# Performance work log

Measured on AMD Instinct MI355X. Metric: run time of the kernel, lower is better.

Reference implementation:

```python
import jax, jax.numpy as jnp
import numpy as np

D = 1024
H = 8
HD = D // H
SCALE = HD ** -0.5


def setup_inputs() -> dict:
    key = jax.random.key(0)
    ks = jax.random.split(key, 12)
    s = 0.02
    return {
        "x": jax.random.normal(ks[0], (4, 2048, D), dtype=jnp.float32),
        "attn_mask": jax.random.randint(ks[1], (2048, 2048), 0, 2, dtype=jnp.int32),
        "qkv_w": jax.random.normal(ks[2], (3 * D, D), dtype=jnp.float32) * s,
        "qkv_b": jnp.zeros((3 * D,), dtype=jnp.float32),
        "q_w": jax.random.normal(ks[3], (D, D), dtype=jnp.float32) * s,
        "q_b": jnp.zeros((D,), dtype=jnp.float32),
        "k_w": jax.random.normal(ks[4], (D, D), dtype=jnp.float32) * s,
        "k_b": jnp.zeros((D,), dtype=jnp.float32),
        "v_w": jax.random.normal(ks[5], (D, D), dtype=jnp.float32) * s,
        "v_b": jnp.zeros((D,), dtype=jnp.float32),
        "out_w": jax.random.normal(ks[6], (D, D), dtype=jnp.float32) * s,
        "out_b": jnp.zeros((D,), dtype=jnp.float32),
    }


def reference(x, attn_mask, qkv_w, qkv_b, q_w, q_b, k_w, k_b, v_w, v_b, out_w, out_b):
    B, S, _ = x.shape
    qkv = x @ qkv_w.T + qkv_b
    q, k, v = jnp.split(qkv, 3, axis=-1)
    # per-stream multi-head projections, then split heads: [B,H,S,HD]
    def heads(t, w, b):
        return (t @ w.T + b).reshape(B, S, H, HD).transpose(0, 2, 1, 3)
    q = heads(q, q_w, q_b)
    k = heads(k, k_w, k_b)
    v = heads(v, v_w, v_b)
    # scaled dot-product attention with masked softmax
    scores = jnp.einsum("bhqd,bhkd->bhqk", q, k) * SCALE
    scores = jnp.where(attn_mask == 1, -jnp.inf, scores)
    attn = jax.nn.softmax(scores, axis=-1)
    o = jnp.einsum("bhqk,bhkd->bhqd", attn, v)
    o = o.transpose(0, 2, 1, 3).reshape(B, S, D)
    return o @ out_w.T + out_b
```

## Files before the change

kernel.cpp:

```cpp
#include <hip/hip_runtime.h>
#include <stdint.h>

typedef unsigned short u16;
typedef unsigned int u32;
typedef unsigned long long u64;
using f32x4 = __attribute__((ext_vector_type(4))) float;
using f32x16 = __attribute__((ext_vector_type(16))) float;
using s16x8 = __attribute__((ext_vector_type(8))) short;
using u16x4 = __attribute__((ext_vector_type(4))) unsigned short;
using u32x4 = __attribute__((ext_vector_type(4))) u32;

static constexpr float kQScale = (float)(0.08838834764831845 * 1.4426950408889634);

__device__ __forceinline__ u16 f2bf(float f) {
  uint32_t u = __float_as_uint(f);
  u += 0x7fffu + ((u >> 16) & 1u);
  return (u16)(u >> 16);
}

__device__ __forceinline__ float fexp2(float x) {
#if __has_builtin(__builtin_amdgcn_exp2f)
  return __builtin_amdgcn_exp2f(x);
#else
  return exp2f(x);
#endif
}

__device__ __forceinline__ u32 cvtpk(float lo, float hi) {
  u32 r;
  asm("v_cvt_pk_bf16_f32 %0, %1, %2" : "=v"(r) : "v"(lo), "v"(hi));
  return r;
}

__device__ __forceinline__ void mfma16(f32x4& d, s16x8 a, s16x8 b) {
  asm volatile("v_mfma_f32_16x16x32_bf16 %0, %1, %2, %0" : "+v"(d) : "v"(a), "v"(b));
}
__device__ __forceinline__ void mfma32(f32x16& d, s16x8 a, s16x8 b) {
  asm volatile("v_mfma_f32_32x32x16_bf16 %0, %1, %2, %0" : "+v"(d) : "v"(a), "v"(b));
}

__device__ __forceinline__ void g2lds16(const void* g, void* l) {
  __builtin_amdgcn_global_load_lds(
      (__attribute__((address_space(1))) void*)(uintptr_t)g,
      (__attribute__((address_space(3))) void*)(uint32_t)(uintptr_t)l, 16, 0, 0);
}

__global__ __launch_bounds__(256) void cvt_f32_bf16(const float* __restrict__ in,
                                                    u16* __restrict__ out, int n) {
  int i = (blockIdx.x * 256 + threadIdx.x) * 4;
  if (i + 3 < n) {
    f32x4 v = *(const f32x4*)(in + i);
    u16x4 o = {f2bf(v.x), f2bf(v.y), f2bf(v.z), f2bf(v.w)};
    *(u16x4*)(out + i) = o;
  }
}

__global__ __launch_bounds__(256) void cvt4(const float* __restrict__ a, const float* __restrict__ b,
                                            const float* __restrict__ c, const float* __restrict__ d,
                                            u16* __restrict__ out) {
  int z = blockIdx.y;
  const float* in = z == 0 ? a : z == 1 ? b : z == 2 ? c : d;
  int i = (blockIdx.x * 256 + threadIdx.x) * 4;
  f32x4 v = *(const f32x4*)(in + i);
  u16x4 o = {f2bf(v.x), f2bf(v.y), f2bf(v.z), f2bf(v.w)};
  *(u16x4*)(out + (size_t)z * 1048576 + i) = o;
}

__global__ __launch_bounds__(256) void transpose_f32_bf16(const float* __restrict__ in,
                                                          u16* __restrict__ out, int R, int C) {
  __shared__ u16 tile[32][33];
  int bx = blockIdx.x, by = blockIdx.y;
  int tx = threadIdx.x & 31, ty = threadIdx.x >> 5;
#pragma unroll
  for (int k = 0; k < 4; ++k)
    tile[ty + k * 8][tx] = f2bf(in[(size_t)(by * 32 + ty + k * 8) * C + bx * 32 + tx]);
  __syncthreads();
#pragma unroll
  for (int k = 0; k < 4; ++k)
    out[(size_t)(bx * 32 + ty + k * 8) * R + by * 32 + tx] = tile[tx][ty + k * 8];
}

__global__ __launch_bounds__(256) void cbias3(const float* __restrict__ qw, const float* __restrict__ kw,
                                              const float* __restrict__ vw, const float* __restrict__ qkvb,
                                              const float* __restrict__ qb, const float* __restrict__ kb,
                                              const float* __restrict__ vb, float* __restrict__ out) {
  int z = blockIdx.y;
  const float* w = z == 0 ? qw : (z == 1 ? kw : vw);
  const float* ba = z == 0 ? qb : (z == 1 ? kb : vb);
  const float* bi = qkvb + z * 1024;
  int o = blockIdx.x * 4 + (threadIdx.x >> 6);
  int lane = threadIdx.x & 63;
  float s = 0.f;
  for (int m = lane; m < 1024; m += 64) s += w[o * 1024 + m] * bi[m];
#pragma unroll
  for (int d = 1; d < 64; d <<= 1) s += __shfl_xor(s, d);
  if (lane == 0) {
    float fin = s + ba[o];
    if (z == 0) fin *= kQScale;
    out[z * 1024 + o] = fin;
  }
}

__global__ __launch_bounds__(256) void pack_mask(const int* __restrict__ m, u64* __restrict__ pm) {
  int row = blockIdx.x;
  int wv = threadIdx.x >> 6, lane = threadIdx.x & 63;
#pragma unroll
  for (int i = 0; i < 8; ++i) {
    int word = wv * 8 + i;
    u64 b = __ballot(m[(size_t)row * 2048 + word * 64 + lane] == 1);
    if (lane == 0) pm[(size_t)row * 32 + word] = b;
  }
}

template <typename OUT_T, bool BIAS_PER_ROW>
__global__ __launch_bounds__(256, 2) void gemm_nt(const u16* __restrict__ A, int lda, long bsA,
                                                  const u16* __restrict__ B, int ldb, long bsB,
                                                  OUT_T* __restrict__ C, int ldc, long bsC,
                                                  const float* __restrict__ bias, long bsBias,
                                                  int NtilesN, int K, float scale_z0) {
  __shared__ __align__(16) u16 As[128 * 64];
  __shared__ __align__(16) u16 Bs[128 * 64];
  const int z = blockIdx.z;
  const float sc = (z == 0) ? scale_z0 : 1.f;
  A += (size_t)z * bsA; B += (size_t)z * bsB; C += (size_t)z * bsC;
  if (bias) bias += (size_t)z * bsBias;
  const int tm = blockIdx.x / NtilesN, tn = blockIdx.x % NtilesN;
  const int tid = threadIdx.x, lane = tid & 63, w = tid >> 6;
  const int wm = w >> 1, wn = w & 1;
  const int q = lane & 15, g = lane >> 4;
  f32x4 acc[4][4] = {};

  const u16* Ab = A + (size_t)(tm * 128 + (tid >> 3)) * lda + ((tid & 7) << 3);
  const u16* Bb = B + (size_t)(tn * 128 + (tid >> 3)) * ldb + ((tid & 7) << 3);
  char* AsW = (char*)As + (w << 10);
  char* BsW = (char*)Bs + (w << 10);

  for (int k0 = 0; k0 < K; k0 += 64) {
#pragma unroll
    for (int it = 0; it < 4; ++it) {
      g2lds16(Ab + (size_t)(it * 32) * lda + k0, AsW + it * 4096);
      g2lds16(Bb + (size_t)(it * 32) * ldb + k0, BsW + it * 4096);
    }
    __syncthreads();
#pragma unroll
    for (int kk = 0; kk < 2; ++kk) {
      s16x8 af[4], bf[4];
#pragma unroll
      for (int i = 0; i < 4; ++i)
        af[i] = *(const s16x8*)((const char*)As + (wm * 64 + i * 16 + q) * 128 + kk * 64 + g * 16);
#pragma unroll
      for (int i = 0; i < 4; ++i)
        bf[i] = *(const s16x8*)((const char*)Bs + (wn * 64 + i * 16 + q) * 128 + kk * 64 + g * 16);
#pragma unroll
      for (int mf = 0; mf < 4; ++mf)
#pragma unroll
        for (int nf = 0; nf < 4; ++nf) mfma16(acc[mf][nf], af[mf], bf[nf]);
    }
    __syncthreads();
  }
  asm volatile("s_nop 7\n\ts_nop 7");
#pragma unroll
  for (int mf = 0; mf < 4; ++mf)
#pragma unroll
    for (int nf = 0; nf < 4; ++nf) {
      const int row = tm * 128 + wm * 64 + mf * 16 + g * 4;
      const int col = tn * 128 + wn * 64 + nf * 16 + q;
      float bc = (!BIAS_PER_ROW && bias) ? bias[col] : 0.f;
#pragma unroll
      for (int r = 0; r < 4; ++r) {
        float v = acc[mf][nf][r] * sc;
        if (bias) v += BIAS_PER_ROW ? bias[row + r] : bc;
        if constexpr (sizeof(OUT_T) == 2)
          C[(size_t)(row + r) * ldc + col] = (OUT_T)f2bf(v);
        else
          C[(size_t)(row + r) * ldc + col] = (OUT_T)v;
      }
    }
}

__global__ __launch_bounds__(256, 2) void attn_fwd(const u16* __restrict__ Qb, const u16* __restrict__ Kb,
                                                   const u16* __restrict__ Vt, const u64* __restrict__ pmask,
                                                   u16* __restrict__ Ob) {
  __shared__ __align__(16) char K_lds[2 * 16384];
  __shared__ __align__(16) char V_lds[2 * 16384];
  __shared__ float l_red[4][32];
  const int n = blockIdx.x;
  const int slot = n >> 3;
  const int grp = (n & 7) * 4 + (slot >> 4);
  const int qt = slot & 15;
  const int h = grp & 7, b = grp >> 3;
  const int tid = threadIdx.x, w = tid >> 6, lane = tid & 63;
  const int ql = lane & 31;
  const int hi = lane >> 5;
  const int q0 = qt * 128;

  s16x8 qf[8];
  const u16* qrow = Qb + (size_t)(b * 2048 + q0 + w * 32 + ql) * 1024 + h * 128 + 8 * hi;
#pragma unroll
  for (int kd = 0; kd < 8; ++kd) qf[kd] = *(const s16x8*)(qrow + 16 * kd);

  f32x16 oacc[4] = {};
  float lp = 0.f;

  const int ksr = tid >> 4, ksc = tid & 15;
  const int vsr = tid >> 3, vsc = tid & 7;
  const int sw = ql & 15;

  auto stageKV = [&](int buf, int s2) {
    const int kv0 = s2 * 64;
    char* kb = K_lds + buf * 16384 + (w << 10);
    char* vb = V_lds + buf * 16384 + (w << 10);
#pragma unroll
    for (int it = 0; it < 4; ++it) {
      int kr = it * 16 + ksr;
      g2lds16(Kb + (size_t)(b * 2048 + kv0 + kr) * 1024 + h * 128 + ((ksc ^ (kr & 15)) << 3),
              kb + it * 4096);
      int vr = it * 32 + vsr;
      g2lds16(Vt + (size_t)(h * 128 + vr) * 8192 + b * 2048 + kv0 + ((vsc ^ (vr & 7)) << 3),
              vb + it * 4096);
    }
  };

  stageKV(0, 0);
  __syncthreads();

  for (int s = 0; s < 32; ++s) {
    const int cur = s & 1;
    if (s + 1 < 32) stageKV(cur ^ 1, s + 1);
    const char* Kc = K_lds + cur * 16384;
    const char* Vc = V_lds + cur * 16384;

    u64 pw = pmask[(size_t)(q0 + w * 32 + ql) * 32 + s];

    f32x16 sacc0 = {}, sacc1 = {};
    __builtin_amdgcn_s_setprio(1);
#pragma unroll
    for (int kd = 0; kd < 8; ++kd) {
      int c = (2 * kd + hi) ^ sw;
      s16x8 kf0 = *(const s16x8*)(Kc + ql * 256 + (c << 4));
      s16x8 kf1 = *(const s16x8*)(Kc + (32 + ql) * 256 + (c << 4));
      mfma32(sacc0, kf0, qf[kd]);
      mfma32(sacc1, kf1, qf[kd]);
    }
    __builtin_amdgcn_s_setprio(0);
    asm volatile("s_nop 7\n\ts_nop 7");

    u32 Wp[8][2];
#pragma unroll
    for (int nt = 0; nt < 2; ++nt) {
      u32 halfm = ((u32)(pw >> (32 * nt))) >> (4 * hi);
#pragma unroll
      for (int t = 0; t < 4; ++t) {
        float e[4];
#pragma unroll
        for (int j = 0; j < 4; ++j) {
          float ev = fexp2((nt == 0 ? sacc0[4 * t + j] : sacc1[4 * t + j]) - 16.f);
          if ((halfm >> (8 * t + j)) & 1u) ev = 0.f;
          e[j] = ev;
          lp += ev;
        }
        Wp[nt * 4 + t][0] = cvtpk(e[0], e[1]);
        Wp[nt * 4 + t][1] = cvtpk(e[2], e[3]);
      }
    }

    s16x8 pa[4];
#pragma unroll
    for (int ks = 0; ks < 4; ++ks) {
      u32 s0 = hi ? Wp[2 * ks][0] : Wp[2 * ks + 1][0];
      u32 s1 = hi ? Wp[2 * ks][1] : Wp[2 * ks + 1][1];
      u32 r0 = (u32)__shfl_xor((int)s0, 32);
      u32 r1 = (u32)__shfl_xor((int)s1, 32);
      u32 o0 = hi ? Wp[2 * ks + 1][0] : Wp[2 * ks][0];
      u32 o1 = hi ? Wp[2 * ks + 1][1] : Wp[2 * ks][1];
      u32x4 wv;
      wv.x = hi ? r0 : o0;
      wv.y = hi ? r1 : o1;
      wv.z = hi ? o0 : r0;
      wv.w = hi ? o1 : r1;
      pa[ks] = __builtin_bit_cast(s16x8, wv);
    }
    asm volatile("s_nop 3");

    __builtin_amdgcn_s_setprio(1);
#pragma unroll
    for (int ks = 0; ks < 4; ++ks) {
#pragma unroll
      for (int dt = 0; dt < 4; ++dt) {
        int vrow = dt * 32 + ql;
        s16x8 vf = *(const s16x8*)(Vc + vrow * 128 + ((((2 * ks + hi)) ^ (vrow & 7)) << 4));
        mfma32(oacc[dt], pa[ks], vf);
      }
    }
    __builtin_amdgcn_s_setprio(0);
    __syncthreads();
  }

  asm volatile("s_nop 7\n\ts_nop 7");
  lp += __shfl_xor(lp, 32);
  if (lane < 32) l_red[w][lane] = 1.f / lp;
  float rl[16];
#pragma unroll
  for (int reg = 0; reg < 16; ++reg)
    rl[reg] = l_red[w][(reg & 3) + 8 * (reg >> 2) + 4 * hi];
#pragma unroll
  for (int dt = 0; dt < 4; ++dt)
#pragma unroll
    for (int reg = 0; reg < 16; ++reg) {
      int qr = (reg & 3) + 8 * (reg >> 2) + 4 * hi;
      size_t trow = (size_t)(b * 2048 + q0 + w * 32 + qr);
      Ob[trow * 1024 + h * 128 + dt * 32 + ql] = f2bf(oacc[dt][reg] * rl[reg]);
    }
}

extern "C" void kernel_launch(void* const* d_in, const int* in_sizes, int n_in,
                              void* d_out, int out_size, void* d_ws, size_t ws_size,
                              hipStream_t stream) {
  (void)in_sizes; (void)n_in; (void)out_size; (void)ws_size;
  const float* x    = (const float*)d_in[0];
  const int*   am   = (const int*)d_in[1];
  const float* qkvw = (const float*)d_in[2];
  const float* qkvb = (const float*)d_in[3];
  const float* qw   = (const float*)d_in[4];
  const float* qb   = (const float*)d_in[5];
  const float* kw   = (const float*)d_in[6];
  const float* kb   = (const float*)d_in[7];
  const float* vw   = (const float*)d_in[8];
  const float* vb   = (const float*)d_in[9];
  const float* ow   = (const float*)d_in[10];
  const float* ob   = (const float*)d_in[11];

  char* p = (char*)d_ws;
  auto take = [&](size_t n) { char* r = p; p += (n + 255) & ~(size_t)255; return r; };
  u16* xb    = (u16*)take(8192ull * 1024 * 2);
  u16* qkvwT = (u16*)take(1024ull * 3072 * 2);
  u16* wb4   = (u16*)take(4ull * 1048576 * 2);
  u16* comb3 = (u16*)take(3ull * 1048576 * 2);
  float* cb3 = (float*)take(3ull * 1024 * 4);
  u16* QK2   = (u16*)take(2ull * 8192 * 1024 * 2);
  u16* V2t   = (u16*)take(8192ull * 1024 * 2);
  u64* pm    = (u64*)take(2048ull * 32 * 8);
  u16* Obuf  = xb;

  cvt_f32_bf16<<<8192, 256, 0, stream>>>(x, xb, 8192 * 1024);
  cvt4<<<dim3(1024, 4), 256, 0, stream>>>(qw, kw, vw, ow, wb4);
  transpose_f32_bf16<<<dim3(32, 96), 256, 0, stream>>>(qkvw, qkvwT, 3072, 1024);
  cbias3<<<dim3(256, 3), 256, 0, stream>>>(qw, kw, vw, qkvb, qb, kb, vb, cb3);

  gemm_nt<u16, false><<<dim3(64, 1, 3), 256, 0, stream>>>(
      wb4, 1024, 1048576, qkvwT, 3072, 1024, comb3, 1024, 1048576, nullptr, 0, 8, 1024, kQScale);
  gemm_nt<u16, false><<<dim3(512, 1, 2), 256, 0, stream>>>(
      xb, 1024, 0, comb3, 1024, 1048576, QK2, 1024, 8192ll * 1024, cb3, 1024, 8, 1024, 1.f);
  gemm_nt<u16, true><<<dim3(512, 1, 1), 256, 0, stream>>>(
      comb3 + 2 * 1048576, 1024, 0, xb, 1024, 0, V2t, 8192, 0, cb3 + 2048, 0, 64, 1024, 1.f);

  pack_mask<<<2048, 256, 0, stream>>>(am, pm);
  attn_fwd<<<512, 256, 0, stream>>>(QK2, QK2 + 8192ull * 1024, V2t, pm, Obuf);

  gemm_nt<float, false><<<dim3(512, 1, 1), 256, 0, stream>>>(
      Obuf, 1024, 0, wb4 + 3 * 1048576, 1024, 0, (float*)d_out, 1024, 0, ob, 0, 8, 1024, 1.f);
}
```

Before: 261.6 us.

## Add 256x256 GEMM for fused QK projection and compute row sums with MFMA

```diff
diff --git a/kernel.cpp b/kernel.cpp
--- a/kernel.cpp
+++ b/kernel.cpp
@@ -38,12 +38,19 @@
 __device__ __forceinline__ void mfma32(f32x16& d, s16x8 a, s16x8 b) {
   asm volatile("v_mfma_f32_32x32x16_bf16 %0, %1, %2, %0" : "+v"(d) : "v"(a), "v"(b));
 }
+__device__ __forceinline__ f32x16 mfma32_z(s16x8 a, s16x8 b) {
+  f32x16 d;
+  asm volatile("v_mfma_f32_32x32x16_bf16 %0, %1, %2, 0" : "=&v"(d) : "v"(a), "v"(b));
+  return d;
+}
 
 __device__ __forceinline__ void g2lds16(const void* g, void* l) {
   __builtin_amdgcn_global_load_lds(
       (__attribute__((address_space(1))) void*)(uintptr_t)g,
       (__attribute__((address_space(3))) void*)(uint32_t)(uintptr_t)l, 16, 0, 0);
 }
+
+#define BAR() asm volatile("s_barrier" ::: "memory")
 
 __global__ __launch_bounds__(256) void cvt_f32_bf16(const float* __restrict__ in,
                                                     u16* __restrict__ out, int n) {
@@ -107,7 +114,7 @@
 #pragma unroll
   for (int i = 0; i < 8; ++i) {
     int word = wv * 8 + i;
-    u64 b = __ballot(m[(size_t)row * 2048 + word * 64 + lane] == 1);
+    u64 b = __ballot(m[(size_t)row * 2048 + word * 64 + lane] == 0);
     if (lane == 0) pm[(size_t)row * 32 + word] = b;
   }
 }
@@ -178,12 +185,126 @@
     }
 }
 
+__global__ __launch_bounds__(512, 1) void gemm256(const u16* __restrict__ A, int lda,
+                                                  const u16* __restrict__ B, int ldb,
+                                                  u16* __restrict__ C, int ldc,
+                                                  const float* __restrict__ bias,
+                                                  int K, int NtN) {
+  __shared__ __align__(16) u16 Als[2][256 * 64];
+  __shared__ __align__(16) u16 Bls[2][256 * 64];
+  const int bid = blockIdx.x;
+  const int cpx = gridDim.x >> 3;
+  const int wgid = (bid & 7) * cpx + (bid >> 3);
+  const int tm = wgid / NtN, tn = wgid % NtN;
+  const int tid = threadIdx.x, lane = tid & 63, w = tid >> 6;
+  const int wm = w >> 2, wn = w & 3;
+  const int q = lane & 15, g = lane >> 4, qk = q & 7;
+  const int nT = K >> 6;
+
+  f32x4 acc[8][4] = {};
+  s16x8 af[4][2], bf[4][2];
+
+  const int srow = tid >> 3, sch = tid & 7;
+  const int gcol = (sch ^ (srow & 7)) << 3;
+  const u16* Abase = A + (size_t)(tm * 256 + srow) * lda + gcol;
+  const u16* Bbase = B + (size_t)(tn * 256 + srow) * ldb + gcol;
+
+  auto stageA = [&](int buf, int kt, int h) {
+    const u16* s0 = Abase + (size_t)(h * 128) * lda + (kt << 6);
+    char* d = (char*)&Als[buf][0] + h * 16384 + (w << 10);
+    g2lds16(s0, d);
+    g2lds16(s0 + (size_t)64 * lda, d + 8192);
+  };
+  auto stageB = [&](int buf, int kt, int h) {
+    const u16* s0 = Bbase + (size_t)(h * 128) * ldb + (kt << 6);
+    char* d = (char*)&Bls[buf][0] + h * 16384 + (w << 10);
+    g2lds16(s0, d);
+    g2lds16(s0 + (size_t)64 * ldb, d + 8192);
+  };
+  auto loadA = [&](const char* base, int mh) {
+#pragma unroll
+    for (int mf = 0; mf < 4; ++mf)
+#pragma unroll
+      for (int kk = 0; kk < 2; ++kk)
+        af[mf][kk] = *(const s16x8*)(base + (mh * 128 + wm * 64 + mf * 16 + q) * 128 +
+                                     ((((kk << 2) + g) ^ qk) << 4));
+  };
+  auto loadB = [&](const char* base, int nh) {
+#pragma unroll
+    for (int nf = 0; nf < 2; ++nf)
+#pragma unroll
+      for (int kk = 0; kk < 2; ++kk)
+        bf[nh * 2 + nf][kk] = *(const s16x8*)(base + (nh * 128 + wn * 32 + nf * 16 + q) * 128 +
+                                              ((((kk << 2) + g) ^ qk) << 4));
+  };
+  auto quad = [&](int mh, int nh) {
+    __builtin_amdgcn_s_setprio(1);
+#pragma unroll
+    for (int mf = 0; mf < 4; ++mf)
+#pragma unroll
+      for (int nf = 0; nf < 2; ++nf)
+#pragma unroll
+        for (int kk = 0; kk < 2; ++kk)
+          mfma16(acc[mh * 4 + mf][nh * 2 + nf], af[mf][kk], bf[nh * 2 + nf][kk]);
+    __builtin_amdgcn_s_setprio(0);
+  };
+
+  stageA(0, 0, 0); stageA(0, 0, 1); stageB(0, 0, 0); stageB(0, 0, 1);
+  const int kt1 = (1 < nT) ? 1 : 0;
+  stageB(1, kt1, 0); stageB(1, kt1, 1);
+  asm volatile("s_waitcnt vmcnt(4)" ::: "memory");
+  BAR();
+
+  for (int kt = 0; kt < nT; ++kt) {
+    const int buf = kt & 1;
+    const char* Ab = (const char*)&Als[buf][0];
+    const char* Bb = (const char*)&Bls[buf][0];
+    const int ktA = (kt + 1 < nT) ? kt + 1 : nT - 1;
+    const int ktB = (kt + 2 < nT) ? kt + 2 : nT - 1;
+    loadA(Ab, 0); loadB(Bb, 0);
+    stageA(buf ^ 1, ktA, 0);
+    BAR();
+    quad(0, 0);
+    BAR();
+    loadB(Bb, 1);
+    stageA(buf ^ 1, ktA, 1);
+    BAR();
+    quad(0, 1);
+    asm volatile("s_waitcnt vmcnt(8)" ::: "memory");
+    BAR();
+    loadA(Ab, 1);
+    stageB(buf, ktB, 0);
+    BAR();
+    quad(1, 0);
+    BAR();
+    stageB(buf, ktB, 1);
+    BAR();
+    quad(1, 1);
+    asm volatile("s_waitcnt vmcnt(6)" ::: "memory");
+    BAR();
+  }
+
+  asm volatile("s_nop 7\n\ts_nop 7");
+#pragma unroll
+  for (int mf = 0; mf < 8; ++mf) {
+    const int row = tm * 256 + (mf >> 2) * 128 + wm * 64 + (mf & 3) * 16 + g * 4;
+#pragma unroll
+    for (int nf = 0; nf < 4; ++nf) {
+      const int col = tn * 256 + (nf >> 1) * 128 + wn * 32 + (nf & 1) * 16 + q;
+      const float bc = bias[col];
+#pragma unroll
+      for (int r = 0; r < 4; ++r)
+        C[(size_t)(row + r) * ldc + col] = f2bf(acc[mf][nf][r] + bc);
+    }
+  }
+}
+
 __global__ __launch_bounds__(256, 2) void attn_fwd(const u16* __restrict__ Qb, const u16* __restrict__ Kb,
-                                                   const u16* __restrict__ Vt, const u64* __restrict__ pmask,
+                                                   int ldq, const u16* __restrict__ Vt,
+                                                   const u64* __restrict__ pmask,
                                                    u16* __restrict__ Ob) {
   __shared__ __align__(16) char K_lds[2 * 16384];
   __shared__ __align__(16) char V_lds[2 * 16384];
-  __shared__ float l_red[4][32];
   const int n = blockIdx.x;
   const int slot = n >> 3;
   const int grp = (n & 7) * 4 + (slot >> 4);
@@ -195,12 +316,15 @@
   const int q0 = qt * 128;
 
   s16x8 qf[8];
-  const u16* qrow = Qb + (size_t)(b * 2048 + q0 + w * 32 + ql) * 1024 + h * 128 + 8 * hi;
+  const u16* qrow = Qb + (size_t)(b * 2048 + q0 + w * 32 + ql) * ldq + h * 128 + 8 * hi;
 #pragma unroll
   for (int kd = 0; kd < 8; ++kd) qf[kd] = *(const s16x8*)(qrow + 16 * kd);
 
+  u32x4 ov = {0x3F803F80u, 0x3F803F80u, 0x3F803F80u, 0x3F803F80u};
+  const s16x8 ones = __builtin_bit_cast(s16x8, ov);
+
   f32x16 oacc[4] = {};
-  float lp = 0.f;
+  f32x16 lacc = {};
 
   const int ksr = tid >> 4, ksc = tid & 15;
   const int vsr = tid >> 3, vsc = tid & 7;
@@ -213,7 +337,7 @@
 #pragma unroll
     for (int it = 0; it < 4; ++it) {
       int kr = it * 16 + ksr;
-      g2lds16(Kb + (size_t)(b * 2048 + kv0 + kr) * 1024 + h * 128 + ((ksc ^ (kr & 15)) << 3),
+      g2lds16(Kb + (size_t)(b * 2048 + kv0 + kr) * ldq + h * 128 + ((ksc ^ (kr & 15)) << 3),
               kb + it * 4096);
       int vr = it * 32 + vsr;
       g2lds16(Vt + (size_t)(h * 128 + vr) * 8192 + b * 2048 + kv0 + ((vsc ^ (vr & 7)) << 3),
@@ -232,15 +356,15 @@
 
     u64 pw = pmask[(size_t)(q0 + w * 32 + ql) * 32 + s];
 
-    f32x16 sacc0 = {}, sacc1 = {};
+    f32x16 sacc0, sacc1;
     __builtin_amdgcn_s_setprio(1);
 #pragma unroll
     for (int kd = 0; kd < 8; ++kd) {
       int c = (2 * kd + hi) ^ sw;
       s16x8 kf0 = *(const s16x8*)(Kc + ql * 256 + (c << 4));
       s16x8 kf1 = *(const s16x8*)(Kc + (32 + ql) * 256 + (c << 4));
-      mfma32(sacc0, kf0, qf[kd]);
-      mfma32(sacc1, kf1, qf[kd]);
+      if (kd == 0) { sacc0 = mfma32_z(kf0, qf[0]); sacc1 = mfma32_z(kf1, qf[0]); }
+      else         { mfma32(sacc0, kf0, qf[kd]);   mfma32(sacc1, kf1, qf[kd]); }
     }
     __builtin_amdgcn_s_setprio(0);
     asm volatile("s_nop 7\n\ts_nop 7");
@@ -248,16 +372,16 @@
     u32 Wp[8][2];
 #pragma unroll
     for (int nt = 0; nt < 2; ++nt) {
-      u32 halfm = ((u32)(pw >> (32 * nt))) >> (4 * hi);
+      u32 halfm = (u32)(pw >> (32 * nt + 4 * hi));
 #pragma unroll
       for (int t = 0; t < 4; ++t) {
         float e[4];
 #pragma unroll
         for (int j = 0; j < 4; ++j) {
-          float ev = fexp2((nt == 0 ? sacc0[4 * t + j] : sacc1[4 * t + j]) - 16.f);
-          if ((halfm >> (8 * t + j)) & 1u) ev = 0.f;
-          e[j] = ev;
-          lp += ev;
+          float ev = fexp2(nt == 0 ? sacc0[4 * t + j] : sacc1[4 * t + j]);
+          int km;
+          asm("v_bfe_i32 %0, %1, %2, 1" : "=v"(km) : "v"(halfm), "n"(8 * t + j));
+          e[j] = __uint_as_float(__float_as_uint(ev) & (u32)km);
         }
         Wp[nt * 4 + t][0] = cvtpk(e[0], e[1]);
         Wp[nt * 4 + t][1] = cvtpk(e[2], e[3]);
@@ -291,25 +415,20 @@
         s16x8 vf = *(const s16x8*)(Vc + vrow * 128 + ((((2 * ks + hi)) ^ (vrow & 7)) << 4));
         mfma32(oacc[dt], pa[ks], vf);
       }
+      mfma32(lacc, pa[ks], ones);
     }
     __builtin_amdgcn_s_setprio(0);
     __syncthreads();
   }
 
   asm volatile("s_nop 7\n\ts_nop 7");
-  lp += __shfl_xor(lp, 32);
-  if (lane < 32) l_red[w][lane] = 1.f / lp;
-  float rl[16];
-#pragma unroll
-  for (int reg = 0; reg < 16; ++reg)
-    rl[reg] = l_red[w][(reg & 3) + 8 * (reg >> 2) + 4 * hi];
 #pragma unroll
   for (int dt = 0; dt < 4; ++dt)
 #pragma unroll
     for (int reg = 0; reg < 16; ++reg) {
       int qr = (reg & 3) + 8 * (reg >> 2) + 4 * hi;
       size_t trow = (size_t)(b * 2048 + q0 + w * 32 + qr);
-      Ob[trow * 1024 + h * 128 + dt * 32 + ql] = f2bf(oacc[dt][reg] * rl[reg]);
+      Ob[trow * 1024 + h * 128 + dt * 32 + ql] = f2bf(oacc[dt][reg] / lacc[reg]);
     }
 }
 
@@ -337,7 +456,7 @@
   u16* wb4   = (u16*)take(4ull * 1048576 * 2);
   u16* comb3 = (u16*)take(3ull * 1048576 * 2);
   float* cb3 = (float*)take(3ull * 1024 * 4);
-  u16* QK2   = (u16*)take(2ull * 8192 * 1024 * 2);
+  u16* QK2   = (u16*)take(8192ull * 2048 * 2);
   u16* V2t   = (u16*)take(8192ull * 1024 * 2);
   u64* pm    = (u64*)take(2048ull * 32 * 8);
   u16* Obuf  = xb;
@@ -349,13 +468,12 @@
 
   gemm_nt<u16, false><<<dim3(64, 1, 3), 256, 0, stream>>>(
       wb4, 1024, 1048576, qkvwT, 3072, 1024, comb3, 1024, 1048576, nullptr, 0, 8, 1024, kQScale);
-  gemm_nt<u16, false><<<dim3(512, 1, 2), 256, 0, stream>>>(
-      xb, 1024, 0, comb3, 1024, 1048576, QK2, 1024, 8192ll * 1024, cb3, 1024, 8, 1024, 1.f);
+  gemm256<<<256, 512, 0, stream>>>(xb, 1024, comb3, 1024, QK2, 2048, cb3, 1024, 8);
   gemm_nt<u16, true><<<dim3(512, 1, 1), 256, 0, stream>>>(
       comb3 + 2 * 1048576, 1024, 0, xb, 1024, 0, V2t, 8192, 0, cb3 + 2048, 0, 64, 1024, 1.f);
 
   pack_mask<<<2048, 256, 0, stream>>>(am, pm);
-  attn_fwd<<<512, 256, 0, stream>>>(QK2, QK2 + 8192ull * 1024, V2t, pm, Obuf);
+  attn_fwd<<<512, 256, 0, stream>>>(QK2, QK2 + 1024, 2048, V2t, pm, Obuf);
 
   gemm_nt<float, false><<<dim3(512, 1, 1), 256, 0, stream>>>(
       Obuf, 1024, 0, wb4 + 3 * 1048576, 1024, 0, (float*)d_out, 1024, 0, ob, 0, 8, 1024, 1.f);
```

Result: faster. 244.8 us (-6.4%).
